# Optimization experiments

Measured on AMD Instinct MI355X. Metric: run time of the kernel, lower is better.

The kernel has to match this reference:

```python
import jax, jax.numpy as jnp
import numpy as np
from jax.scipy.special import i0

# Module config (init_kwargs). sector_width only affects CUDA tiling, not math.
OSF = 2
KERNEL_WIDTH = 3
IMG_DIM = 320
B, M = 8, 200000


def setup_inputs() -> dict:
    key = jax.random.key(0)
    k1, k2, k3, k4 = jax.random.split(key, 4)
    x_re = jax.random.normal(k1, (B, IMG_DIM, IMG_DIM), jnp.float32)
    x_im = jax.random.normal(k2, (B, IMG_DIM, IMG_DIM), jnp.float32)
    # normalized k-space trajectory in [-0.5, 0.5) (gpuNUFFT convention)
    traj = jax.random.uniform(k3, (B, 2, M), jnp.float32, -0.5, 0.5)
    # density compensation weights, strictly positive
    dcf = jax.random.uniform(k4, (B, M), jnp.float32, 0.01, 1.0)
    return {"x_re": x_re, "x_im": x_im, "traj": traj, "dcf": dcf}


def _kb(d, W, beta):
    # Kaiser-Bessel gridding kernel, support |d| <= W/2 (d in oversampled grid units)
    t = jnp.clip(1.0 - (2.0 * d / W) ** 2, 0.0, None)
    return jnp.where(jnp.abs(d) <= W / 2.0, i0(beta * jnp.sqrt(t)), 0.0)


def _deapod_1d(N, G, W, beta):
    # Fourier transform of the KB kernel, sampled at image positions n/G
    xs = (jnp.arange(N, dtype=jnp.float32) - N // 2) / G
    arg = beta ** 2 - (jnp.pi * W * xs) ** 2
    s = jnp.sqrt(jnp.abs(arg))
    return jnp.where(arg > 0, jnp.sinh(s) / s, jnp.sinc(s / jnp.pi))


def _nufft_forward(x_re, x_im, traj, dcf):
    N, G, L = IMG_DIM, OSF * IMG_DIM, KERNEL_WIDTH
    W = float(KERNEL_WIDTH)
    # Beatty et al. optimal KB shape parameter
    beta = jnp.pi * np.sqrt((W / OSF) ** 2 * (OSF - 0.5) ** 2 - 0.8)

    # 1) deapodize image
    c = _deapod_1d(N, G, W, beta)  # [N]
    img = (x_re + 1j * x_im) / (c[:, None] * c[None, :])

    # 2) zero-pad to oversampled grid and FFT (centered)
    pad = (G - N) // 2
    img_p = jnp.pad(img, ((0, 0), (pad, pad), (pad, pad)))
    kgrid = jnp.fft.fftshift(
        jnp.fft.fft2(jnp.fft.ifftshift(img_p, axes=(1, 2)), axes=(1, 2)),
        axes=(1, 2)) / G  # [B,G,G]

    # 3) KB interpolation onto non-uniform samples
    coords = (traj + 0.5) * G                         # [B,2,M] in [0,G)
    offs = jnp.arange(L, dtype=jnp.float32)
    base = jnp.floor(coords - (L - 1) / 2.0)          # [B,2,M]
    idx = base[..., None] + offs                      # [B,2,M,L]
    d = coords[..., None] - idx                       # [B,2,M,L]
    w = _kb(d, W, beta)                               # [B,2,M,L]
    wx, wy = w[:, 0], w[:, 1]                         # x=cols, y=rows
    ix = idx[:, 0].astype(jnp.int32) % G              # [B,M,L]
    iy = idx[:, 1].astype(jnp.int32) % G
    flat = iy[:, :, :, None] * G + ix[:, :, None, :]  # [B,M,L,L]
    weights = wy[:, :, :, None] * wx[:, :, None, :]   # [B,M,L,L]
    vals = jax.vmap(lambda g, i: g[i])(kgrid.reshape(kgrid.shape[0], G * G), flat)
    k = jnp.sum(vals * weights.astype(vals.dtype), axis=(-1, -2))  # [B,M]

    # 4) density compensation (sqrt(dcf) weighting of forward samples)
    k = k * jnp.sqrt(dcf)
    return jnp.stack([k.real, k.imag], axis=-1)  # [B,M,2]


def reference(x_re, x_im, traj, dcf):
    return _nufft_forward(x_re, x_im, traj, dcf)
```

## Files before the change

### kernel.cpp

```cpp
#include <hip/hip_runtime.h>
#include <math.h>

#define GDIM 640
#define NDIM 320
#define NB 8
#define NM 200000
#define PI_F 3.14159265358979323846f

__device__ __forceinline__ float bessel_i0f(float x) {
    if (x < 3.75f) {
        float t = x * (1.0f / 3.75f);
        t *= t;
        return 1.0f + t * (3.5156229f + t * (3.0899424f + t * (1.2067492f +
                     t * (0.2659732f + t * (0.0360768f + t * 0.0045813f)))));
    }
    float t = 3.75f / x;
    float p = 0.39894228f + t * (0.01328592f + t * (0.00225319f + t * (-0.00157565f +
              t * (0.00916281f + t * (-0.02057706f + t * (0.02635537f +
              t * (-0.01647633f + t * 0.00392377f)))))));
    return p * __expf(x) * rsqrtf(x);
}

__device__ __forceinline__ float deapod_c(int i, float beta2) {
    float xs = (float)(i - NDIM / 2) * (1.0f / (float)GDIM);
    float p = PI_F * 3.0f * xs;
    float arg = beta2 - p * p;
    float s = sqrtf(fabsf(arg));
    if (arg > 0.0f) return sinhf(s) / s;
    return (s < 1e-12f) ? 1.0f : sinf(s) / s;
}

__device__ __forceinline__ float kbw(float d, float beta) {
    if (fabsf(d) > 1.5f) return 0.0f;
    float u = d * (2.0f / 3.0f);
    float t = 1.0f - u * u;
    t = fmaxf(t, 0.0f);
    return bessel_i0f(beta * sqrtf(t));
}

__device__ __forceinline__ void fft640_core(float2* lds, float2* lds2, int tid) {
    if (tid < 128) {
        const int bb = tid;
        float2 xa[5];
#pragma unroll
        for (int a = 0; a < 5; ++a) xa[a] = lds[a * 128 + bb];
        const float c5[5] = {1.0f, 0.30901699f, -0.80901699f, -0.80901699f, 0.30901699f};
        const float s5[5] = {0.0f, -0.95105652f, -0.58778525f, 0.58778525f, 0.95105652f};
#pragma unroll
        for (int k1 = 0; k1 < 5; ++k1) {
            float2 acc = xa[0];
#pragma unroll
            for (int a = 1; a < 5; ++a) {
                int j = (a * k1) % 5;
                acc.x += xa[a].x * c5[j] - xa[a].y * s5[j];
                acc.y += xa[a].x * s5[j] + xa[a].y * c5[j];
            }
            float ang = -2.0f * PI_F * (float)(bb * k1) * (1.0f / 640.0f);
            float sw, cw;
            __sincosf(ang, &sw, &cw);
            float2 r;
            r.x = acc.x * cw - acc.y * sw;
            r.y = acc.x * sw + acc.y * cw;
            lds2[k1 * 128 + bb] = r;
        }
    }
    __syncthreads();

    const int f = tid >> 6;
    const int j = tid & 63;
    float2* arr = lds2 + f * 128;
#pragma unroll
    for (int h = 64; h >= 1; h >>= 1) {
        int g = j / h;
        int jj = j - g * h;
        int p = g * 2 * h + jj;
        float2 u = arr[p];
        float2 v = arr[p + h];
        float2 s = make_float2(u.x + v.x, u.y + v.y);
        float2 d = make_float2(u.x - v.x, u.y - v.y);
        float ang = -PI_F * (float)jj / (float)h;
        float sw, cw;
        __sincosf(ang, &sw, &cw);
        arr[p] = s;
        arr[p + h] = make_float2(d.x * cw - d.y * sw, d.x * sw + d.y * cw);
        __syncthreads();
    }

#pragma unroll
    for (int half = 0; half < 2; ++half) {
        int k2 = j + 64 * half;
        int src = f * 128 + (int)(__brev((unsigned)k2) >> 25);
        int k = f + 5 * k2;
        int ks = (k >= 320) ? (k - 320) : (k + 320);
        lds[ks] = lds2[src];
    }
}

__global__ __launch_bounds__(320) void pass_a(const float* __restrict__ x_re,
                                              const float* __restrict__ x_im,
                                              float2* __restrict__ buf1c,
                                              float beta2) {
    __shared__ float2 lds[640];
    __shared__ float2 lds2[640];
    const int b = blockIdx.y;
    const int r = blockIdx.x;
    const int tid = threadIdx.x;

    const int ry = (r < 160) ? (r + 160) : (r - 160);
    const float cy = deapod_c(ry, beta2);
    const float scale = 1.0f / (cy * (float)GDIM);

    for (int i = tid; i < GDIM; i += 320) {
        int xx = (i >= 320) ? (i - 320) : (i + 320);
        float2 v = make_float2(0.0f, 0.0f);
        if (xx >= 160 && xx < 480) {
            int rx = xx - 160;
            float cx = deapod_c(rx, beta2);
            float sc = scale / cx;
            size_t off = ((size_t)b * NDIM + ry) * NDIM + rx;
            v.x = x_re[off] * sc;
            v.y = x_im[off] * sc;
        }
        lds[i] = v;
    }
    __syncthreads();

    fft640_core(lds, lds2, tid);
    __syncthreads();

    float2* dst = buf1c + ((size_t)b * NDIM + r) * GDIM;
    for (int i = tid; i < GDIM; i += 320) dst[i] = lds[i];
}

__global__ __launch_bounds__(320) void pass_b(const float2* __restrict__ buf1c,
                                              float2* __restrict__ kbuf) {
    __shared__ float2 lds[640];
    __shared__ float2 lds2[640];
    const int b = blockIdx.y;
    const int raw = blockIdx.x;
    const int kxs = (raw & 7) * 80 + (raw >> 3);
    const int tid = threadIdx.x;

    for (int i = tid; i < GDIM; i += 320) {
        float2 v = make_float2(0.0f, 0.0f);
        int yc = (i < 160) ? i : ((i >= 480) ? (i - 320) : -1);
        if (yc >= 0) v = buf1c[((size_t)b * NDIM + yc) * GDIM + kxs];
        lds[i] = v;
    }
    __syncthreads();

    fft640_core(lds, lds2, tid);
    __syncthreads();

    float2* dst = kbuf + ((size_t)b * GDIM + kxs) * GDIM;
    for (int i = tid; i < GDIM; i += 320) dst[i] = lds[i];
}

#define GBLK_PER_B ((NM + 255) / 256)
__global__ __launch_bounds__(256) void gather_kernel(const float* __restrict__ traj,
                                                     const float* __restrict__ dcf,
                                                     const float2* __restrict__ kbuf,
                                                     float2* __restrict__ out,
                                                     float beta) {
    const int bid = blockIdx.x;
    const int b = bid & 7;
    const int m = (bid >> 3) * 256 + threadIdx.x;
    if (m >= NM) return;

    const float tx = traj[((size_t)b * 2 + 0) * NM + m];
    const float ty = traj[((size_t)b * 2 + 1) * NM + m];
    const float cx = (tx + 0.5f) * (float)GDIM;
    const float cy = (ty + 0.5f) * (float)GDIM;
    const float bx = floorf(cx - 1.0f);
    const float by = floorf(cy - 1.0f);

    float wx[3], wy[3];
    int ix[3], iy[3];
#pragma unroll
    for (int l = 0; l < 3; ++l) {
        float dx = cx - (bx + (float)l);
        float dy = cy - (by + (float)l);
        wx[l] = kbw(dx, beta);
        wy[l] = kbw(dy, beta);
        int i = (int)bx + l;
        i %= GDIM; if (i < 0) i += GDIM;
        ix[l] = i;
        int jj = (int)by + l;
        jj %= GDIM; if (jj < 0) jj += GDIM;
        iy[l] = jj;
    }

    float accx = 0.0f, accy = 0.0f;
#pragma unroll
    for (int lx = 0; lx < 3; ++lx) {
        const float2* row = kbuf + ((size_t)b * GDIM + ix[lx]) * GDIM;
        const float wxl = wx[lx];
#pragma unroll
        for (int ly = 0; ly < 3; ++ly) {
            float w = wy[ly] * wxl;
            float2 v = row[iy[ly]];
            accx += v.x * w;
            accy += v.y * w;
        }
    }
    const float s = sqrtf(dcf[(size_t)b * NM + m]);
    out[(size_t)b * NM + m] = make_float2(accx * s, accy * s);
}

extern "C" void kernel_launch(void* const* d_in, const int* in_sizes, int n_in,
                              void* d_out, int out_size, void* d_ws, size_t ws_size,
                              hipStream_t stream) {
    const float* x_re = (const float*)d_in[0];
    const float* x_im = (const float*)d_in[1];
    const float* traj = (const float*)d_in[2];
    const float* dcf  = (const float*)d_in[3];

    float2* buf1c = (float2*)d_ws;
    float2* kbuf  = buf1c + (size_t)NB * NDIM * GDIM;

    const double beta_d = M_PI * sqrt((1.5 * 1.5) * (1.5 * 1.5) - 0.8);
    const float beta = (float)beta_d;
    const float beta2 = (float)(beta_d * beta_d);

    dim3 gridA(NDIM, NB);
    pass_a<<<gridA, 320, 0, stream>>>(x_re, x_im, buf1c, beta2);

    dim3 gridB(GDIM, NB);
    pass_b<<<gridB, 320, 0, stream>>>(buf1c, kbuf);

    gather_kernel<<<GBLK_PER_B * NB, 256, 0, stream>>>(traj, dcf, kbuf,
                                                       (float2*)d_out, beta);
}
```

Before: 78.25 us.

## Pad k-space grid with wraparound halo and vectorize gather loads

```diff
diff --git a/kernel.cpp b/kernel.cpp
--- a/kernel.cpp
+++ b/kernel.cpp
@@ -5,6 +5,8 @@
 #define NDIM 320
 #define NB 8
 #define NM 200000
+#define KROWS 643
+#define KSTRIDE 644
 #define PI_F 3.14159265358979323846f
 
 __device__ __forceinline__ float bessel_i0f(float x) {
@@ -38,7 +40,16 @@
     return bessel_i0f(beta * sqrtf(t));
 }
 
-__device__ __forceinline__ void fft640_core(float2* lds, float2* lds2, int tid) {
+__device__ __forceinline__ void build_tw(float2* tw, int tid) {
+    for (int i = tid; i < 640; i += 320) {
+        float sw, cw;
+        __sincosf(-2.0f * PI_F * (float)i * (1.0f / 640.0f), &sw, &cw);
+        tw[i] = make_float2(cw, sw);
+    }
+}
+
+__device__ __forceinline__ void fft640_core(float2* lds, float2* lds2,
+                                            const float2* tw, int tid) {
     if (tid < 128) {
         const int bb = tid;
         float2 xa[5];
@@ -55,12 +66,10 @@
                 acc.x += xa[a].x * c5[j] - xa[a].y * s5[j];
                 acc.y += xa[a].x * s5[j] + xa[a].y * c5[j];
             }
-            float ang = -2.0f * PI_F * (float)(bb * k1) * (1.0f / 640.0f);
-            float sw, cw;
-            __sincosf(ang, &sw, &cw);
+            float2 w = tw[bb * k1];
             float2 r;
-            r.x = acc.x * cw - acc.y * sw;
-            r.y = acc.x * sw + acc.y * cw;
+            r.x = acc.x * w.x - acc.y * w.y;
+            r.y = acc.x * w.y + acc.y * w.x;
             lds2[k1 * 128 + bb] = r;
         }
     }
@@ -78,11 +87,9 @@
         float2 v = arr[p + h];
         float2 s = make_float2(u.x + v.x, u.y + v.y);
         float2 d = make_float2(u.x - v.x, u.y - v.y);
-        float ang = -PI_F * (float)jj / (float)h;
-        float sw, cw;
-        __sincosf(ang, &sw, &cw);
+        float2 w = tw[jj * (320 / h)];
         arr[p] = s;
-        arr[p + h] = make_float2(d.x * cw - d.y * sw, d.x * sw + d.y * cw);
+        arr[p + h] = make_float2(d.x * w.x - d.y * w.y, d.x * w.y + d.y * w.x);
         __syncthreads();
     }
 
@@ -102,9 +109,12 @@
                                               float beta2) {
     __shared__ float2 lds[640];
     __shared__ float2 lds2[640];
+    __shared__ float2 tw[640];
     const int b = blockIdx.y;
     const int r = blockIdx.x;
     const int tid = threadIdx.x;
+
+    build_tw(tw, tid);
 
     const int ry = (r < 160) ? (r + 160) : (r - 160);
     const float cy = deapod_c(ry, beta2);
@@ -125,7 +135,7 @@
     }
     __syncthreads();
 
-    fft640_core(lds, lds2, tid);
+    fft640_core(lds, lds2, tw, tid);
     __syncthreads();
 
     float2* dst = buf1c + ((size_t)b * NDIM + r) * GDIM;
@@ -134,26 +144,52 @@
 
 __global__ __launch_bounds__(320) void pass_b(const float2* __restrict__ buf1c,
                                               float2* __restrict__ kbuf) {
-    __shared__ float2 lds[640];
+    __shared__ float2 colsT[4][648];
     __shared__ float2 lds2[640];
+    __shared__ float2 tw[640];
     const int b = blockIdx.y;
-    const int raw = blockIdx.x;
-    const int kxs = (raw & 7) * 80 + (raw >> 3);
+    const int kxs0 = blockIdx.x * 4;
     const int tid = threadIdx.x;
 
-    for (int i = tid; i < GDIM; i += 320) {
-        float2 v = make_float2(0.0f, 0.0f);
-        int yc = (i < 160) ? i : ((i >= 480) ? (i - 320) : -1);
-        if (yc >= 0) v = buf1c[((size_t)b * NDIM + yc) * GDIM + kxs];
-        lds[i] = v;
-    }
-    __syncthreads();
-
-    fft640_core(lds, lds2, tid);
-    __syncthreads();
-
-    float2* dst = kbuf + ((size_t)b * GDIM + kxs) * GDIM;
-    for (int i = tid; i < GDIM; i += 320) dst[i] = lds[i];
+    build_tw(tw, tid);
+
+    for (int base = 0; base < NDIM; base += 80) {
+        int r = base + (tid >> 2);
+        int c = tid & 3;
+        float2 v = buf1c[((size_t)b * NDIM + r) * GDIM + kxs0 + c];
+        int y = (r < 160) ? r : (r + 320);
+        colsT[c][y] = v;
+    }
+    for (int i = tid; i < 1280; i += 320) {
+        colsT[i & 3][160 + (i >> 2)] = make_float2(0.0f, 0.0f);
+    }
+    __syncthreads();
+
+    float2* kbb = kbuf + (size_t)b * KROWS * KSTRIDE;
+
+#pragma unroll
+    for (int c = 0; c < 4; ++c) {
+        fft640_core(&colsT[c][0], lds2, tw, tid);
+        __syncthreads();
+
+        const int kxs = kxs0 + c;
+        int prs[2];
+        int nduprow = 1;
+        prs[0] = kxs + 1;
+        if (kxs == 639) { prs[1] = 0;   nduprow = 2; }
+        if (kxs == 0)   { prs[1] = 641; nduprow = 2; }
+        if (kxs == 1)   { prs[1] = 642; nduprow = 2; }
+        for (int rr = 0; rr < nduprow; ++rr) {
+            float2* dst = kbb + (size_t)prs[rr] * KSTRIDE;
+            for (int i = tid; i < GDIM; i += 320) dst[1 + i] = colsT[c][i];
+            if (tid == 0) {
+                dst[0]   = colsT[c][639];
+                dst[641] = colsT[c][0];
+                dst[642] = colsT[c][1];
+            }
+        }
+        __syncthreads();
+    }
 }
 
 #define GBLK_PER_B ((NM + 255) / 256)
@@ -171,37 +207,45 @@
     const float ty = traj[((size_t)b * 2 + 1) * NM + m];
     const float cx = (tx + 0.5f) * (float)GDIM;
     const float cy = (ty + 0.5f) * (float)GDIM;
-    const float bx = floorf(cx - 1.0f);
-    const float by = floorf(cy - 1.0f);
+    const int bxi = (int)floorf(cx - 1.0f);
+    const int byi = (int)floorf(cy - 1.0f);
+    const float fx = cx - (float)bxi;
+    const float fy = cy - (float)byi;
+
+    const float2* __restrict__ kb = kbuf + (size_t)b * KROWS * KSTRIDE;
+    const int pc0 = byi + 1;
+    const int odd = pc0 & 1;
+
+    float4 A[3], Bv[3];
+#pragma unroll
+    for (int lx = 0; lx < 3; ++lx) {
+        size_t e = ((size_t)(bxi + 1 + lx) * KSTRIDE + (size_t)pc0) & ~(size_t)1;
+        const float4* p = (const float4*)(kb + e);
+        A[lx] = p[0];
+        Bv[lx] = p[1];
+    }
 
     float wx[3], wy[3];
-    int ix[3], iy[3];
 #pragma unroll
     for (int l = 0; l < 3; ++l) {
-        float dx = cx - (bx + (float)l);
-        float dy = cy - (by + (float)l);
-        wx[l] = kbw(dx, beta);
-        wy[l] = kbw(dy, beta);
-        int i = (int)bx + l;
-        i %= GDIM; if (i < 0) i += GDIM;
-        ix[l] = i;
-        int jj = (int)by + l;
-        jj %= GDIM; if (jj < 0) jj += GDIM;
-        iy[l] = jj;
+        wx[l] = kbw(fx - (float)l, beta);
+        wy[l] = kbw(fy - (float)l, beta);
     }
 
     float accx = 0.0f, accy = 0.0f;
 #pragma unroll
     for (int lx = 0; lx < 3; ++lx) {
-        const float2* row = kbuf + ((size_t)b * GDIM + ix[lx]) * GDIM;
-        const float wxl = wx[lx];
-#pragma unroll
-        for (int ly = 0; ly < 3; ++ly) {
-            float w = wy[ly] * wxl;
-            float2 v = row[iy[ly]];
-            accx += v.x * w;
-            accy += v.y * w;
-        }
+        float t0x = odd ? A[lx].z : A[lx].x;
+        float t0y = odd ? A[lx].w : A[lx].y;
+        float t1x = odd ? Bv[lx].x : A[lx].z;
+        float t1y = odd ? Bv[lx].y : A[lx].w;
+        float t2x = odd ? Bv[lx].z : Bv[lx].x;
+        float t2y = odd ? Bv[lx].w : Bv[lx].y;
+        const float w0 = wx[lx] * wy[0];
+        const float w1 = wx[lx] * wy[1];
+        const float w2 = wx[lx] * wy[2];
+        accx += t0x * w0 + t1x * w1 + t2x * w2;
+        accy += t0y * w0 + t1y * w1 + t2y * w2;
     }
     const float s = sqrtf(dcf[(size_t)b * NM + m]);
     out[(size_t)b * NM + m] = make_float2(accx * s, accy * s);
@@ -225,7 +269,7 @@
     dim3 gridA(NDIM, NB);
     pass_a<<<gridA, 320, 0, stream>>>(x_re, x_im, buf1c, beta2);
 
-    dim3 gridB(GDIM, NB);
+    dim3 gridB(GDIM / 4, NB);
     pass_b<<<gridB, 320, 0, stream>>>(buf1c, kbuf);
 
     gather_kernel<<<GBLK_PER_B * NB, 256, 0, stream>>>(traj, dcf, kbuf,
```

Result: slower. 82.12 us (+5.0%).
